# Kernel optimization log

Measured on AMD Instinct MI355X. Metric: run time of the kernel, lower is better.

The kernel has to match this reference:

```python
import jax, jax.numpy as jnp
import numpy as np

DIM, DEPTH, HEADS, DIM_HEAD, MLP_DIM = 512, 6, 8, 64, 2048
INNER = HEADS * DIM_HEAD
EPS = 1e-5


def _layernorm(x, s, b):
    mu = jnp.mean(x, axis=-1, keepdims=True)
    var = jnp.mean(jnp.square(x - mu), axis=-1, keepdims=True)
    return (x - mu) * jax.lax.rsqrt(var + EPS) * s + b


def setup_inputs() -> dict:
    key = jax.random.key(0)
    ks = jax.random.split(key, 12)
    d = {
        "x": jax.random.normal(ks[0], (8, 1024, DIM), dtype=jnp.float32),
        "ln1_s": jnp.ones((DEPTH, DIM), jnp.float32),
        "ln1_b": jnp.zeros((DEPTH, DIM), jnp.float32),
        "w_qkv": jax.random.normal(ks[1], (DEPTH, DIM, 3 * INNER), dtype=jnp.float32) * (DIM ** -0.5),
        "w_out": jax.random.normal(ks[2], (DEPTH, INNER, DIM), dtype=jnp.float32) * (INNER ** -0.5),
        "b_out": jnp.zeros((DEPTH, DIM), jnp.float32),
        "ln2_s": jnp.ones((DEPTH, DIM), jnp.float32),
        "ln2_b": jnp.zeros((DEPTH, DIM), jnp.float32),
        "w1": jax.random.normal(ks[3], (DEPTH, DIM, MLP_DIM), dtype=jnp.float32) * (DIM ** -0.5),
        "b1": jnp.zeros((DEPTH, MLP_DIM), jnp.float32),
        "w2": jax.random.normal(ks[4], (DEPTH, MLP_DIM, DIM), dtype=jnp.float32) * (MLP_DIM ** -0.5),
        "b2": jnp.zeros((DEPTH, DIM), jnp.float32),
    }
    return d


def reference(x, ln1_s, ln1_b, w_qkv, w_out, b_out, ln2_s, ln2_b, w1, b1, w2, b2):
    b, n, _ = x.shape
    scale = DIM_HEAD ** -0.5
    for i in range(DEPTH):
        # --- PreNorm Attention with residual ---
        h = _layernorm(x, ln1_s[i], ln1_b[i])
        qkv = h @ w_qkv[i]                                  # [b, n, 3*inner]
        q, k, v = jnp.split(qkv, 3, axis=-1)
        q = q.reshape(b, n, HEADS, DIM_HEAD)
        k = k.reshape(b, n, HEADS, DIM_HEAD)
        v = v.reshape(b, n, HEADS, DIM_HEAD)
        dots = jnp.einsum('bihd,bjhd->bhij', q, k) * scale  # [b, h, n, n]
        attn = jax.nn.softmax(dots, axis=-1)
        out = jnp.einsum('bhij,bjhd->bihd', attn, v).reshape(b, n, INNER)
        x = out @ w_out[i] + b_out[i] + x
        # --- PreNorm FeedForward with residual ---
        h = _layernorm(x, ln2_s[i], ln2_b[i])
        h = jax.nn.gelu(h @ w1[i] + b1[i], approximate=False)
        x = h @ w2[i] + b2[i] + x
    return x
```

## Files before the change

### kernel.cpp

```cpp
#include <hip/hip_runtime.h>
#include <cstdint>
#include <cstddef>

#define M_TOK 8192
#define DIMM  512
#define HEADS 8
#define DH    64
#define MLPD  2048
#define DEPTH 6

typedef unsigned short u16;
typedef unsigned int   u32;
typedef __attribute__((ext_vector_type(8))) short short8;
typedef __attribute__((ext_vector_type(4))) float f32x4;

__device__ __forceinline__ float bf2f(u16 u){ return __uint_as_float(((u32)u) << 16); }
__device__ __forceinline__ u16 f2bf(float f){
    u32 x = __float_as_uint(f);
    u32 r = x + 0x7fffu + ((x >> 16) & 1u);
    return (u16)(r >> 16);
}
__device__ __forceinline__ u32 cvt_pk_bf16(float a, float b){
    u32 r;
    asm("v_cvt_pk_bf16_f32 %0, %1, %2" : "=v"(r) : "v"(a), "v"(b));
    return r;
}
__device__ __forceinline__ void async16(const u16* g, u16* l){
    __builtin_amdgcn_global_load_lds(
        (const __attribute__((address_space(1))) void*)(uintptr_t)(const void*)g,
        (__attribute__((address_space(3))) void*)(u32)(uintptr_t)(void*)l,
        16, 0, 0);
}

__global__ void k_transpose_cvt(const float* __restrict__ in, u16* __restrict__ out, int R, int C){
    __shared__ u16 tile[32][33];
    size_t zoff = (size_t)blockIdx.z * R * C;
    in += zoff; out += zoff;
    int c0 = blockIdx.x * 32, r0 = blockIdx.y * 32;
    int tx = threadIdx.x, ty = threadIdx.y;
    #pragma unroll
    for (int i = 0; i < 32; i += 8)
        tile[ty + i][tx] = f2bf(in[(size_t)(r0 + ty + i) * C + c0 + tx]);
    __syncthreads();
    #pragma unroll
    for (int i = 0; i < 32; i += 8)
        out[(size_t)(c0 + ty + i) * R + r0 + tx] = tile[tx][ty + i];
}

__global__ __launch_bounds__(256) void k_layernorm(const float* __restrict__ x,
                                                   const float* __restrict__ s,
                                                   const float* __restrict__ b,
                                                   u16* __restrict__ out){
    int row = blockIdx.x * 4 + (threadIdx.x >> 6);
    int lane = threadIdx.x & 63;
    const float* xp = x + (size_t)row * DIMM + lane * 8;
    float v[8];
    #pragma unroll
    for (int c = 0; c < 8; c++) v[c] = xp[c];
    float sum = 0.f, sq = 0.f;
    #pragma unroll
    for (int c = 0; c < 8; c++){ sum += v[c]; sq += v[c] * v[c]; }
    #pragma unroll
    for (int m = 32; m >= 1; m >>= 1){
        sum += __shfl_xor(sum, m);
        sq  += __shfl_xor(sq,  m);
    }
    float mu  = sum * (1.f / DIMM);
    float var = sq * (1.f / DIMM) - mu * mu;
    float rs  = rsqrtf(var + 1e-5f);
    u16* op = out + (size_t)row * DIMM + lane * 8;
    #pragma unroll
    for (int c = 0; c < 8; c++){
        int col = lane * 8 + c;
        op[c] = f2bf((v[c] - mu) * rs * s[col] + b[col]);
    }
}

__device__ __forceinline__ float gelu_exact(float v){
    return 0.5f * v * (1.f + erff(v * 0.70710678118654752f));
}

#define LDT64 72

template<int MODE>
__global__ __launch_bounds__(256) void k_gemm128b(const u16* __restrict__ A,
                                                  const u16* __restrict__ Bt,
                                                  const float* __restrict__ bias,
                                                  u16* __restrict__ Cout,
                                                  int M, int N, int K){
    __shared__ u16 As[2][128 * 64];
    __shared__ u16 Bs[2][128 * 64];
    int m0 = blockIdx.y * 128, n0 = blockIdx.x * 128;
    int t = threadIdx.x;
    int w = t >> 6, lane = t & 63;
    int mi = lane & 15, quad = lane >> 4;
    int wr = w >> 1, wc = w & 1;

    int grow = lane >> 3, gcol = (lane & 7) * 8;
    const u16* agl = A  + (size_t)(m0 + w * 32 + grow) * K + gcol;
    const u16* bgl = Bt + (size_t)(n0 + w * 32 + grow) * K + gcol;

    f32x4 acc[4][4];
    #pragma unroll
    for (int mt = 0; mt < 4; mt++)
        #pragma unroll
        for (int nt = 0; nt < 4; nt++) acc[mt][nt] = (f32x4){0.f, 0.f, 0.f, 0.f};

    int nt_k = K >> 6;
    {
        u16* asl = &As[0][(w * 32) * 64];
        u16* bsl = &Bs[0][(w * 32) * 64];
        #pragma unroll
        for (int i = 0; i < 4; i++){
            async16(agl + (size_t)(i * 8) * K, asl + i * 8 * 64);
            async16(bgl + (size_t)(i * 8) * K, bsl + i * 8 * 64);
        }
    }
    __syncthreads();

    for (int td = 0; td < nt_k; td++){
        int cur = td & 1;
        if (td + 1 < nt_k){
            int k0 = (td + 1) << 6;
            u16* asl = &As[cur ^ 1][(w * 32) * 64];
            u16* bsl = &Bs[cur ^ 1][(w * 32) * 64];
            #pragma unroll
            for (int i = 0; i < 4; i++){
                async16(agl + (size_t)(i * 8) * K + k0, asl + i * 8 * 64);
                async16(bgl + (size_t)(i * 8) * K + k0, bsl + i * 8 * 64);
            }
        }
        const u16* Ab = &As[cur][0];
        const u16* Bb = &Bs[cur][0];
        #pragma unroll
        for (int kk = 0; kk < 64; kk += 32){
            short8 af[4], bf[4];
            #pragma unroll
            for (int mt = 0; mt < 4; mt++)
                af[mt] = *(const short8*)&Ab[(wr * 64 + mt * 16 + mi) * 64 + kk + quad * 8];
            #pragma unroll
            for (int nt = 0; nt < 4; nt++)
                bf[nt] = *(const short8*)&Bb[(wc * 64 + nt * 16 + mi) * 64 + kk + quad * 8];
            #pragma unroll
            for (int mt = 0; mt < 4; mt++)
                #pragma unroll
                for (int nt = 0; nt < 4; nt++)
                    acc[mt][nt] = __builtin_amdgcn_mfma_f32_16x16x32_bf16(af[mt], bf[nt], acc[mt][nt], 0, 0, 0);
        }
        __syncthreads();
    }

    float bv[4];
    if (MODE == 1){
        #pragma unroll
        for (int nt = 0; nt < 4; nt++) bv[nt] = bias[n0 + wc * 64 + nt * 16 + mi];
    }
    u16* cs = ((u16*)As) + w * 16 * LDT64;
    int erow = lane >> 2, ecol = (lane & 3) * 16;
    #pragma unroll
    for (int mt = 0; mt < 4; mt++){
        #pragma unroll
        for (int nt = 0; nt < 4; nt++)
            #pragma unroll
            for (int r = 0; r < 4; r++){
                float v = acc[mt][nt][r];
                if (MODE == 1) v = gelu_exact(v + bv[nt]);
                cs[(quad * 4 + r) * LDT64 + nt * 16 + mi] = f2bf(v);
            }
        uint4 c0 = *(const uint4*)&cs[erow * LDT64 + ecol];
        uint4 c1 = *(const uint4*)&cs[erow * LDT64 + ecol + 8];
        u16* cp = Cout + (size_t)(m0 + wr * 64 + mt * 16 + erow) * N + n0 + wc * 64 + ecol;
        *(uint4*)cp       = c0;
        *(uint4*)(cp + 8) = c1;
    }
}

__global__ __launch_bounds__(256) void k_gemm64_res(const u16* __restrict__ A,
                                                    const u16* __restrict__ Bt,
                                                    const float* __restrict__ bias,
                                                    float* __restrict__ xres,
                                                    int M, int N, int K){
    __shared__ u16 As[2][64 * 64];
    __shared__ u16 Bs[2][64 * 64];
    int m0 = blockIdx.y * 64, n0 = blockIdx.x * 64;
    int t = threadIdx.x;
    int w = t >> 6, lane = t & 63;
    int mi = lane & 15, quad = lane >> 4;

    int grow = lane >> 3, gcol = (lane & 7) * 8;
    const u16* agl = A  + (size_t)(m0 + w * 16 + grow) * K + gcol;
    const u16* bgl = Bt + (size_t)(n0 + w * 16 + grow) * K + gcol;

    f32x4 acc[4];
    #pragma unroll
    for (int tt = 0; tt < 4; tt++) acc[tt] = (f32x4){0.f, 0.f, 0.f, 0.f};

    int nt_k = K >> 6;
    {
        u16* asl = &As[0][(w * 16) * 64];
        u16* bsl = &Bs[0][(w * 16) * 64];
        #pragma unroll
        for (int i = 0; i < 2; i++){
            async16(agl + (size_t)(i * 8) * K, asl + i * 8 * 64);
            async16(bgl + (size_t)(i * 8) * K, bsl + i * 8 * 64);
        }
    }
    __syncthreads();

    for (int td = 0; td < nt_k; td++){
        int cur = td & 1;
        if (td + 1 < nt_k){
            int k0 = (td + 1) << 6;
            u16* asl = &As[cur ^ 1][(w * 16) * 64];
            u16* bsl = &Bs[cur ^ 1][(w * 16) * 64];
            #pragma unroll
            for (int i = 0; i < 2; i++){
                async16(agl + (size_t)(i * 8) * K + k0, asl + i * 8 * 64);
                async16(bgl + (size_t)(i * 8) * K + k0, bsl + i * 8 * 64);
            }
        }
        const u16* Ab = &As[cur][0];
        const u16* Bb = &Bs[cur][0];
        short8 af0 = *(const short8*)&Ab[(w * 16 + mi) * 64 + quad * 8];
        short8 af1 = *(const short8*)&Ab[(w * 16 + mi) * 64 + quad * 8 + 32];
        #pragma unroll
        for (int tt = 0; tt < 4; tt++){
            short8 bf0 = *(const short8*)&Bb[(tt * 16 + mi) * 64 + quad * 8];
            short8 bf1 = *(const short8*)&Bb[(tt * 16 + mi) * 64 + quad * 8 + 32];
            acc[tt] = __builtin_amdgcn_mfma_f32_16x16x32_bf16(af0, bf0, acc[tt], 0, 0, 0);
            acc[tt] = __builtin_amdgcn_mfma_f32_16x16x32_bf16(af1, bf1, acc[tt], 0, 0, 0);
        }
        __syncthreads();
    }

    float bv[4];
    #pragma unroll
    for (int tt = 0; tt < 4; tt++) bv[tt] = bias[n0 + tt * 16 + mi];
    float* cs = (w < 2) ? ((float*)As + w * 16 * LDT64)
                        : ((float*)Bs + (w - 2) * 16 * LDT64);
    #pragma unroll
    for (int tt = 0; tt < 4; tt++)
        #pragma unroll
        for (int r = 0; r < 4; r++)
            cs[(quad * 4 + r) * LDT64 + tt * 16 + mi] = acc[tt][r] + bv[tt];
    int erow = lane >> 2, ecol = (lane & 3) * 16;
    float* xp = xres + (size_t)(m0 + w * 16 + erow) * N + n0 + ecol;
    #pragma unroll
    for (int j = 0; j < 4; j++){
        float4 cv = *(const float4*)&cs[erow * LDT64 + ecol + j * 4];
        float4 xv = *(const float4*)(xp + j * 4);
        xv.x += cv.x; xv.y += cv.y; xv.z += cv.z; xv.w += cv.w;
        *(float4*)(xp + j * 4) = xv;
    }
}

#define LDK 72
#define C1_LOG2E 0.18033688011112042f
#define C2_LOG2E 11.541560327111707f

__global__ __launch_bounds__(256) void k_flash(const u16* __restrict__ qkv, u16* __restrict__ out){
    __shared__ u16 Ks[64 * LDK];
    __shared__ u16 Vt[80 * LDK];
    __shared__ u16 Ps[4][32 * LDK];
    int wg = (blockIdx.x & 7) * 64 + (blockIdx.x >> 3);
    int qt = wg & 7, h = (wg >> 3) & 7, b = wg >> 6;
    int t = threadIdx.x;
    int w = t >> 6, lane = t & 63;
    int mi = lane & 15, quad = lane >> 4;

    for (int i = t; i < 16 * 64; i += 256){
        int d = i >> 6, kk = i & 63;
        Vt[(64 + d) * LDK + kk] = 0x3F80;
    }

    const u16* base = qkv + ((size_t)b * 1024) * 1536;
    int hoff = h * 64;

    short8 qf[2][2];
    #pragma unroll
    for (int qh = 0; qh < 2; qh++){
        int qrow = qt * 128 + w * 32 + qh * 16 + mi;
        const u16* qp = base + (size_t)qrow * 1536 + hoff + quad * 8;
        qf[qh][0] = *(const short8*)(qp);
        qf[qh][1] = *(const short8*)(qp + 32);
    }

    f32x4 o[2][4];
    f32x4 lacc[2];
    #pragma unroll
    for (int qh = 0; qh < 2; qh++){
        #pragma unroll
        for (int nb = 0; nb < 4; nb++) o[qh][nb] = (f32x4){0.f, 0.f, 0.f, 0.f};
        lacc[qh] = (f32x4){0.f, 0.f, 0.f, 0.f};
    }

    int kkey = t >> 2, kseg = t & 3;
    const u16* kgp = base + (size_t)kkey * 1536 + 512 + hoff + kseg * 16;
    int vkey = lane, vdg = w;
    const u16* vgp = base + (size_t)vkey * 1536 + 1024 + hoff + vdg * 16;

    uint4 kv0 = *(const uint4*)(kgp);
    uint4 kv1 = *(const uint4*)(kgp + 8);
    uint4 vv0 = *(const uint4*)(vgp);
    uint4 vv1 = *(const uint4*)(vgp + 8);

    for (int kt = 0; kt < 16; kt++){
        __syncthreads();
        *(uint4*)&Ks[kkey * LDK + kseg * 16]     = kv0;
        *(uint4*)&Ks[kkey * LDK + kseg * 16 + 8] = kv1;
        u16 vtmp[16];
        *(uint4*)&vtmp[0] = vv0;
        *(uint4*)&vtmp[8] = vv1;
        #pragma unroll
        for (int i = 0; i < 16; i++)
            Vt[(vdg * 16 + i) * LDK + vkey] = vtmp[i];
        __syncthreads();

        if (kt < 15){
            size_t koff = (size_t)(kt + 1) * 64 * 1536;
            kv0 = *(const uint4*)(kgp + koff);
            kv1 = *(const uint4*)(kgp + koff + 8);
            vv0 = *(const uint4*)(vgp + koff);
            vv1 = *(const uint4*)(vgp + koff + 8);
        }

        short8 kb[4][2];
        #pragma unroll
        for (int nb = 0; nb < 4; nb++){
            kb[nb][0] = *(const short8*)&Ks[(nb * 16 + mi) * LDK + quad * 8];
            kb[nb][1] = *(const short8*)&Ks[(nb * 16 + mi) * LDK + quad * 8 + 32];
        }
        #pragma unroll
        for (int qh = 0; qh < 2; qh++){
            #pragma unroll
            for (int nb = 0; nb < 4; nb++){
                f32x4 z = (f32x4){0.f, 0.f, 0.f, 0.f};
                z = __builtin_amdgcn_mfma_f32_16x16x32_bf16(qf[qh][0], kb[nb][0], z, 0, 0, 0);
                z = __builtin_amdgcn_mfma_f32_16x16x32_bf16(qf[qh][1], kb[nb][1], z, 0, 0, 0);
                float e0 = exp2f(fmaf(z[0], C1_LOG2E, -C2_LOG2E));
                float e1 = exp2f(fmaf(z[1], C1_LOG2E, -C2_LOG2E));
                float e2 = exp2f(fmaf(z[2], C1_LOG2E, -C2_LOG2E));
                float e3 = exp2f(fmaf(z[3], C1_LOG2E, -C2_LOG2E));
                u32 p01 = cvt_pk_bf16(e0, e1);
                u32 p23 = cvt_pk_bf16(e2, e3);
                u16* pp = &Ps[w][(qh * 16 + quad * 4) * LDK + nb * 16 + mi];
                pp[0]       = (u16)p01;
                pp[LDK]     = (u16)(p01 >> 16);
                pp[2 * LDK] = (u16)p23;
                pp[3 * LDK] = (u16)(p23 >> 16);
            }
        }
        short8 vb[4][2], lb[2];
        #pragma unroll
        for (int nb = 0; nb < 4; nb++){
            vb[nb][0] = *(const short8*)&Vt[(nb * 16 + mi) * LDK + quad * 8];
            vb[nb][1] = *(const short8*)&Vt[(nb * 16 + mi) * LDK + quad * 8 + 32];
        }
        lb[0] = *(const short8*)&Vt[(64 + mi) * LDK + quad * 8];
        lb[1] = *(const short8*)&Vt[(64 + mi) * LDK + quad * 8 + 32];
        #pragma unroll
        for (int qh = 0; qh < 2; qh++){
            const short8 a0 = *(const short8*)&Ps[w][(qh * 16 + mi) * LDK + quad * 8];
            const short8 a1 = *(const short8*)&Ps[w][(qh * 16 + mi) * LDK + quad * 8 + 32];
            #pragma unroll
            for (int nb = 0; nb < 4; nb++){
                o[qh][nb] = __builtin_amdgcn_mfma_f32_16x16x32_bf16(a0, vb[nb][0], o[qh][nb], 0, 0, 0);
                o[qh][nb] = __builtin_amdgcn_mfma_f32_16x16x32_bf16(a1, vb[nb][1], o[qh][nb], 0, 0, 0);
            }
            lacc[qh] = __builtin_amdgcn_mfma_f32_16x16x32_bf16(a0, lb[0], lacc[qh], 0, 0, 0);
            lacc[qh] = __builtin_amdgcn_mfma_f32_16x16x32_bf16(a1, lb[1], lacc[qh], 0, 0, 0);
        }
    }
    #pragma unroll
    for (int qh = 0; qh < 2; qh++){
        float invl[4];
        #pragma unroll
        for (int r = 0; r < 4; r++) invl[r] = 1.f / lacc[qh][r];
        u16* op = out + ((size_t)b * 1024 + qt * 128 + w * 32 + qh * 16) * 512 + hoff;
        #pragma unroll
        for (int nb = 0; nb < 4; nb++){
            u32 c01 = cvt_pk_bf16(o[qh][nb][0] * invl[0], o[qh][nb][1] * invl[1]);
            u32 c23 = cvt_pk_bf16(o[qh][nb][2] * invl[2], o[qh][nb][3] * invl[3]);
            u16* cp = op + (size_t)(quad * 4) * 512 + nb * 16 + mi;
            cp[0]       = (u16)c01;
            cp[512]     = (u16)(c01 >> 16);
            cp[2 * 512] = (u16)c23;
            cp[3 * 512] = (u16)(c23 >> 16);
        }
    }
}

extern "C" void kernel_launch(void* const* d_in, const int* in_sizes, int n_in,
                              void* d_out, int out_size, void* d_ws, size_t ws_size,
                              hipStream_t stream){
    const float* x_in  = (const float*)d_in[0];
    const float* ln1_s = (const float*)d_in[1];
    const float* ln1_b = (const float*)d_in[2];
    const float* w_qkv = (const float*)d_in[3];
    const float* w_out = (const float*)d_in[4];
    const float* b_out = (const float*)d_in[5];
    const float* ln2_s = (const float*)d_in[6];
    const float* ln2_b = (const float*)d_in[7];
    const float* w1    = (const float*)d_in[8];
    const float* b1    = (const float*)d_in[9];
    const float* w2    = (const float*)d_in[10];
    const float* b2    = (const float*)d_in[11];
    float* out = (float*)d_out;

    char* ws = (char*)d_ws;
    float* x_f32 = (float*)ws;   ws += (size_t)M_TOK * DIMM * 4;
    u16* bufA    = (u16*)ws;     ws += (size_t)M_TOK * DIMM * 2;
    u16* bufB    = (u16*)ws;     ws += (size_t)M_TOK * MLPD * 2;
    u16* wbase   = (u16*)ws;
    size_t per_layer_w = (size_t)(1536 + 512 + 2048 + 2048) * 512;

    size_t used_big = (size_t)(ws - (char*)d_ws) + per_layer_w * 2 * DEPTH;
    bool big = (ws_size >= used_big);

    u16* ln_out   = bufA;
    u16* attn_out = bufA;
    u16* qkv      = bufB;
    u16* mlp_h    = bufB;

    size_t x_bytes = (size_t)M_TOK * DIMM * sizeof(float);
    hipMemcpyAsync(x_f32, x_in, x_bytes, hipMemcpyDeviceToDevice, stream);

    const size_t off_qkv = 0;
    const size_t off_out = (size_t)1536 * 512;
    const size_t off_w1  = off_out + (size_t)512 * 512;
    const size_t off_w2  = off_w1 + (size_t)2048 * 512;

    if (big){
        k_transpose_cvt<<<dim3(48, 16, 6), dim3(32, 8), 0, stream>>>(w_qkv, wbase + off_qkv * DEPTH, 512, 1536);
        k_transpose_cvt<<<dim3(16, 16, 6), dim3(32, 8), 0, stream>>>(w_out, wbase + off_out * DEPTH, 512, 512);
        k_transpose_cvt<<<dim3(64, 16, 6), dim3(32, 8), 0, stream>>>(w1,    wbase + off_w1  * DEPTH, 512, 2048);
        k_transpose_cvt<<<dim3(16, 64, 6), dim3(32, 8), 0, stream>>>(w2,    wbase + off_w2  * DEPTH, 2048, 512);
    }

    for (int i = 0; i < DEPTH; i++){
        u16 *wqkvT, *woutT, *w1T, *w2T;
        if (big){
            wqkvT = wbase + off_qkv * DEPTH + (size_t)i * 1536 * 512;
            woutT = wbase + off_out * DEPTH + (size_t)i * 512 * 512;
            w1T   = wbase + off_w1  * DEPTH + (size_t)i * 2048 * 512;
            w2T   = wbase + off_w2  * DEPTH + (size_t)i * 512 * 2048;
        } else {
            wqkvT = wbase + off_qkv; woutT = wbase + off_out;
            w1T   = wbase + off_w1;  w2T   = wbase + off_w2;
            k_transpose_cvt<<<dim3(48, 16), dim3(32, 8), 0, stream>>>(w_qkv + (size_t)i * 512 * 1536, wqkvT, 512, 1536);
            k_transpose_cvt<<<dim3(16, 16), dim3(32, 8), 0, stream>>>(w_out + (size_t)i * 512 * 512,  woutT, 512, 512);
            k_transpose_cvt<<<dim3(64, 16), dim3(32, 8), 0, stream>>>(w1    + (size_t)i * 512 * 2048, w1T,   512, 2048);
            k_transpose_cvt<<<dim3(16, 64), dim3(32, 8), 0, stream>>>(w2    + (size_t)i * 2048 * 512, w2T,   2048, 512);
        }

        k_layernorm<<<dim3(M_TOK / 4), dim3(256), 0, stream>>>(x_f32, ln1_s + i * 512, ln1_b + i * 512, ln_out);
        k_gemm128b<0><<<dim3(12, 64), dim3(256), 0, stream>>>(ln_out, wqkvT, nullptr, qkv,
                                                              M_TOK, 1536, 512);
        k_flash<<<dim3(512), dim3(256), 0, stream>>>(qkv, attn_out);
        k_gemm64_res<<<dim3(8, 128), dim3(256), 0, stream>>>(attn_out, woutT, b_out + i * 512, x_f32,
                                                             M_TOK, 512, 512);
        k_layernorm<<<dim3(M_TOK / 4), dim3(256), 0, stream>>>(x_f32, ln2_s + i * 512, ln2_b + i * 512, ln_out);
        k_gemm128b<1><<<dim3(16, 64), dim3(256), 0, stream>>>(ln_out, w1T, b1 + i * 2048, mlp_h,
                                                              M_TOK, 2048, 512);
        k_gemm64_res<<<dim3(8, 128), dim3(256), 0, stream>>>(mlp_h, w2T, b2 + i * 512, x_f32,
                                                             M_TOK, 512, 2048);
    }
    hipMemcpyAsync(out, x_f32, x_bytes, hipMemcpyDeviceToDevice, stream);
}
```

Baseline: 1.263 ms.

## Use 128x128 tiles for residual GEMMs and add XCD-aware block swizzle

Replaces the 64x64 residual GEMM kernel with a 128x128-tile version in which each wave computes a 64x64 sub-tile (4x4 MFMA accumulators), raising arithmetic intensity and LDS reuse for the w_out and w2 projections. Also adds an XCD swizzle that remaps block indices so consecutive row-blocks land on the same XCD, improving L2 locality for both GEMM kernels. The larger tile shrinks the residual GEMM grid from 1024 to 256 blocks, which may underfill the 256 CUs and lengthen the K=2048 tail.

```diff
diff --git a/kernel.cpp b/kernel.cpp
--- a/kernel.cpp
+++ b/kernel.cpp
@@ -30,6 +30,16 @@
         (const __attribute__((address_space(1))) void*)(uintptr_t)(const void*)g,
         (__attribute__((address_space(3))) void*)(u32)(uintptr_t)(void*)l,
         16, 0, 0);
+}
+__device__ __forceinline__ void xcd_swizzle(int& bx, int& by){
+    int nbx = gridDim.x, nby = gridDim.y;
+    if ((nby & 7) == 0){
+        int i = by * nbx + bx;
+        int xcd = i & 7, j = i >> 3, ypg = nby >> 3;
+        int yq = j / nbx;
+        by = xcd * ypg + yq;
+        bx = j - yq * nbx;
+    }
 }
 
 __global__ void k_transpose_cvt(const float* __restrict__ in, u16* __restrict__ out, int R, int C){
@@ -90,7 +100,9 @@
                                                   int M, int N, int K){
     __shared__ u16 As[2][128 * 64];
     __shared__ u16 Bs[2][128 * 64];
-    int m0 = blockIdx.y * 128, n0 = blockIdx.x * 128;
+    int bx = blockIdx.x, by = blockIdx.y;
+    xcd_swizzle(bx, by);
+    int m0 = by * 128, n0 = bx * 128;
     int t = threadIdx.x;
     int w = t >> 6, lane = t & 63;
     int mi = lane & 15, quad = lane >> 4;
@@ -175,32 +187,37 @@
     }
 }
 
-__global__ __launch_bounds__(256) void k_gemm64_res(const u16* __restrict__ A,
-                                                    const u16* __restrict__ Bt,
-                                                    const float* __restrict__ bias,
-                                                    float* __restrict__ xres,
-                                                    int M, int N, int K){
-    __shared__ u16 As[2][64 * 64];
-    __shared__ u16 Bs[2][64 * 64];
-    int m0 = blockIdx.y * 64, n0 = blockIdx.x * 64;
+__global__ __launch_bounds__(256) void k_gemm128_res(const u16* __restrict__ A,
+                                                     const u16* __restrict__ Bt,
+                                                     const float* __restrict__ bias,
+                                                     float* __restrict__ xres,
+                                                     int M, int N, int K){
+    __shared__ u16 As[2][128 * 64];
+    __shared__ u16 Bs[2][128 * 64];
+    int bx = blockIdx.x, by = blockIdx.y;
+    xcd_swizzle(bx, by);
+    int m0 = by * 128, n0 = bx * 128;
     int t = threadIdx.x;
     int w = t >> 6, lane = t & 63;
     int mi = lane & 15, quad = lane >> 4;
+    int wr = w >> 1, wc = w & 1;
 
     int grow = lane >> 3, gcol = (lane & 7) * 8;
-    const u16* agl = A  + (size_t)(m0 + w * 16 + grow) * K + gcol;
-    const u16* bgl = Bt + (size_t)(n0 + w * 16 + grow) * K + gcol;
-
-    f32x4 acc[4];
-    #pragma unroll
-    for (int tt = 0; tt < 4; tt++) acc[tt] = (f32x4){0.f, 0.f, 0.f, 0.f};
+    const u16* agl = A  + (size_t)(m0 + w * 32 + grow) * K + gcol;
+    const u16* bgl = Bt + (size_t)(n0 + w * 32 + grow) * K + gcol;
+
+    f32x4 acc[4][4];
+    #pragma unroll
+    for (int mt = 0; mt < 4; mt++)
+        #pragma unroll
+        for (int nt = 0; nt < 4; nt++) acc[mt][nt] = (f32x4){0.f, 0.f, 0.f, 0.f};
 
     int nt_k = K >> 6;
     {
-        u16* asl = &As[0][(w * 16) * 64];
-        u16* bsl = &Bs[0][(w * 16) * 64];
-        #pragma unroll
-        for (int i = 0; i < 2; i++){
+        u16* asl = &As[0][(w * 32) * 64];
+        u16* bsl = &Bs[0][(w * 32) * 64];
+        #pragma unroll
+        for (int i = 0; i < 4; i++){
             async16(agl + (size_t)(i * 8) * K, asl + i * 8 * 64);
             async16(bgl + (size_t)(i * 8) * K, bsl + i * 8 * 64);
         }
@@ -211,46 +228,54 @@
         int cur = td & 1;
         if (td + 1 < nt_k){
             int k0 = (td + 1) << 6;
-            u16* asl = &As[cur ^ 1][(w * 16) * 64];
-            u16* bsl = &Bs[cur ^ 1][(w * 16) * 64];
-            #pragma unroll
-            for (int i = 0; i < 2; i++){
+            u16* asl = &As[cur ^ 1][(w * 32) * 64];
+            u16* bsl = &Bs[cur ^ 1][(w * 32) * 64];
+            #pragma unroll
+            for (int i = 0; i < 4; i++){
                 async16(agl + (size_t)(i * 8) * K + k0, asl + i * 8 * 64);
                 async16(bgl + (size_t)(i * 8) * K + k0, bsl + i * 8 * 64);
             }
         }
         const u16* Ab = &As[cur][0];
         const u16* Bb = &Bs[cur][0];
-        short8 af0 = *(const short8*)&Ab[(w * 16 + mi) * 64 + quad * 8];
-        short8 af1 = *(const short8*)&Ab[(w * 16 + mi) * 64 + quad * 8 + 32];
-        #pragma unroll
-        for (int tt = 0; tt < 4; tt++){
-            short8 bf0 = *(const short8*)&Bb[(tt * 16 + mi) * 64 + quad * 8];
-            short8 bf1 = *(const short8*)&Bb[(tt * 16 + mi) * 64 + quad * 8 + 32];
-            acc[tt] = __builtin_amdgcn_mfma_f32_16x16x32_bf16(af0, bf0, acc[tt], 0, 0, 0);
-            acc[tt] = __builtin_amdgcn_mfma_f32_16x16x32_bf16(af1, bf1, acc[tt], 0, 0, 0);
+        #pragma unroll
+        for (int kk = 0; kk < 64; kk += 32){
+            short8 af[4], bf[4];
+            #pragma unroll
+            for (int mt = 0; mt < 4; mt++)
+                af[mt] = *(const short8*)&Ab[(wr * 64 + mt * 16 + mi) * 64 + kk + quad * 8];
+            #pragma unroll
+            for (int nt = 0; nt < 4; nt++)
+                bf[nt] = *(const short8*)&Bb[(wc * 64 + nt * 16 + mi) * 64 + kk + quad * 8];
+            #pragma unroll
+            for (int mt = 0; mt < 4; mt++)
+                #pragma unroll
+                for (int nt = 0; nt < 4; nt++)
+                    acc[mt][nt] = __builtin_amdgcn_mfma_f32_16x16x32_bf16(af[mt], bf[nt], acc[mt][nt], 0, 0, 0);
         }
         __syncthreads();
     }
 
     float bv[4];
     #pragma unroll
-    for (int tt = 0; tt < 4; tt++) bv[tt] = bias[n0 + tt * 16 + mi];
-    float* cs = (w < 2) ? ((float*)As + w * 16 * LDT64)
-                        : ((float*)Bs + (w - 2) * 16 * LDT64);
-    #pragma unroll
-    for (int tt = 0; tt < 4; tt++)
-        #pragma unroll
-        for (int r = 0; r < 4; r++)
-            cs[(quad * 4 + r) * LDT64 + tt * 16 + mi] = acc[tt][r] + bv[tt];
+    for (int nt = 0; nt < 4; nt++) bv[nt] = bias[n0 + wc * 64 + nt * 16 + mi];
+    float* cs = ((float*)As) + w * 16 * LDT64;
     int erow = lane >> 2, ecol = (lane & 3) * 16;
-    float* xp = xres + (size_t)(m0 + w * 16 + erow) * N + n0 + ecol;
-    #pragma unroll
-    for (int j = 0; j < 4; j++){
-        float4 cv = *(const float4*)&cs[erow * LDT64 + ecol + j * 4];
-        float4 xv = *(const float4*)(xp + j * 4);
-        xv.x += cv.x; xv.y += cv.y; xv.z += cv.z; xv.w += cv.w;
-        *(float4*)(xp + j * 4) = xv;
+    #pragma unroll
+    for (int mt = 0; mt < 4; mt++){
+        #pragma unroll
+        for (int nt = 0; nt < 4; nt++)
+            #pragma unroll
+            for (int r = 0; r < 4; r++)
+                cs[(quad * 4 + r) * LDT64 + nt * 16 + mi] = acc[mt][nt][r] + bv[nt];
+        float* xp = xres + (size_t)(m0 + wr * 64 + mt * 16 + erow) * N + n0 + wc * 64 + ecol;
+        #pragma unroll
+        for (int j = 0; j < 4; j++){
+            float4 cv = *(const float4*)&cs[erow * LDT64 + ecol + j * 4];
+            float4 xv = *(const float4*)(xp + j * 4);
+            xv.x += cv.x; xv.y += cv.y; xv.z += cv.z; xv.w += cv.w;
+            *(float4*)(xp + j * 4) = xv;
+        }
     }
 }
 
@@ -457,12 +482,12 @@
         k_gemm128b<0><<<dim3(12, 64), dim3(256), 0, stream>>>(ln_out, wqkvT, nullptr, qkv,
                                                               M_TOK, 1536, 512);
         k_flash<<<dim3(512), dim3(256), 0, stream>>>(qkv, attn_out);
-        k_gemm64_res<<<dim3(8, 128), dim3(256), 0, stream>>>(attn_out, woutT, b_out + i * 512, x_f32,
+        k_gemm128_res<<<dim3(4, 64), dim3(256), 0, stream>>>(attn_out, woutT, b_out + i * 512, x_f32,
                                                              M_TOK, 512, 512);
         k_layernorm<<<dim3(M_TOK / 4), dim3(256), 0, stream>>>(x_f32, ln2_s + i * 512, ln2_b + i * 512, ln_out);
         k_gemm128b<1><<<dim3(16, 64), dim3(256), 0, stream>>>(ln_out, w1T, b1 + i * 2048, mlp_h,
                                                               M_TOK, 2048, 512);
-        k_gemm64_res<<<dim3(8, 128), dim3(256), 0, stream>>>(mlp_h, w2T, b2 + i * 512, x_f32,
+        k_gemm128_res<<<dim3(4, 64), dim3(256), 0, stream>>>(mlp_h, w2T, b2 + i * 512, x_f32,
                                                              M_TOK, 512, 2048);
     }
     hipMemcpyAsync(out, x_f32, x_bytes, hipMemcpyDeviceToDevice, stream);
```

New measurement: 1.195 ms. -5.4%, faster.
